# Optimization experiments

Measured on AMD Instinct MI355X. Metric: run time of the kernel, lower is better.

## Reference

```python
import jax, jax.numpy as jnp
import numpy as np

N, E, G, D, H = 50000, 800000, 64, 64, 256  # nodes, edges, graphs, feat dim, mlp hidden


def _mlp(x, W1, b1, W2, b2):
    return jax.nn.relu(x @ W1 + b1) @ W2 + b2


def _param(key, fan_in, fan_out):
    return jax.random.normal(key, (fan_in, fan_out), dtype=jnp.float32) * (1.0 / np.sqrt(fan_in))


def setup_inputs() -> dict:
    key = jax.random.key(0)
    ks = jax.random.split(key, 16)
    inp = {
        "nf": jax.random.normal(ks[0], (N, D), dtype=jnp.float32),
        "ef": jax.random.normal(ks[1], (E, D), dtype=jnp.float32),
        "u": jax.random.normal(ks[2], (G, D), dtype=jnp.float32),
        "src": jax.random.randint(ks[3], (E,), 0, N, dtype=jnp.int32),
        "dst": jax.random.randint(ks[4], (E,), 0, N, dtype=jnp.int32),
        "node_gid": jnp.sort(jax.random.randint(ks[5], (N,), 0, G, dtype=jnp.int32)),
        "edge_gid": jnp.sort(jax.random.randint(ks[6], (E,), 0, G, dtype=jnp.int32)),
        # edge_model: in = De + 2*Dn + Du = 4D
        "eW1": _param(ks[7], 4 * D, H), "eb1": jnp.zeros((H,), jnp.float32),
        "eW2": _param(ks[8], H, D),     "eb2": jnp.zeros((D,), jnp.float32),
        # node_model: in = De + Dn + Du = 3D
        "nW1": _param(ks[9], 3 * D, H), "nb1": jnp.zeros((H,), jnp.float32),
        "nW2": _param(ks[10], H, D),    "nb2": jnp.zeros((D,), jnp.float32),
        # global_model: in = De + Dn + Du = 3D
        "gW1": _param(ks[11], 3 * D, H), "gb1": jnp.zeros((H,), jnp.float32),
        "gW2": _param(ks[12], H, D),     "gb2": jnp.zeros((D,), jnp.float32),
    }
    return inp


def reference(nf, ef, u, src, dst, node_gid, edge_gid,
              eW1, eb1, eW2, eb2, nW1, nb1, nW2, nb2, gW1, gb1, gW2, gb2):
    # --- edge update: cat([ef, src_nf, dst_nf, u_per_edge]) -> edge MLP ---
    u_e = u[edge_gid]                                   # [E, D] (repeat_interleave by batch_num_edges)
    em_in = jnp.concatenate([ef, nf[src], nf[dst], u_e], axis=-1)  # [E, 4D]
    ef_new = _mlp(em_in, eW1, eb1, eW2, eb2)            # [E, D]

    # --- message = copy_e, reduce = sum at destination nodes ---
    agg_m = jax.ops.segment_sum(ef_new, dst, num_segments=N)       # [N, D]

    # --- node update: cat([agg_m, nf, u_per_node]) -> node MLP ---
    u_n = u[node_gid]                                   # [N, D]
    nm_in = jnp.concatenate([agg_m, nf, u_n], axis=-1)  # [N, 3D]
    nf_new = _mlp(nm_in, nW1, nb1, nW2, nb2)            # [N, D]

    # --- global update: per-graph sum readouts of updated edge/node feats ---
    e_aggr = jax.ops.segment_sum(ef_new, edge_gid, num_segments=G)  # [G, D]
    n_aggr = jax.ops.segment_sum(nf_new, node_gid, num_segments=G)  # [G, D]
    gm_in = jnp.concatenate([e_aggr, n_aggr, u], axis=-1)           # [G, 3D]
    u_new = _mlp(gm_in, gW1, gb1, gW2, gb2)             # [G, D]

    return nf_new, ef_new, u_new
```

## Files before the change

### kernel.cpp

```cpp
#include <hip/hip_runtime.h>
#include <stdint.h>
#include <stddef.h>

#define NN 50000
#define EE 800000
#define GG 64
#define DD 64
#define HH 256

typedef float f32x4 __attribute__((ext_vector_type(4)));
typedef short s16x8 __attribute__((ext_vector_type(8)));
typedef short s16x4 __attribute__((ext_vector_type(4)));

__device__ __forceinline__ short f2bf(float f) {
    union { float f; unsigned u; } v; v.f = f;
    return (short)((v.u + 0x7FFFu + ((v.u >> 16) & 1u)) >> 16);
}

__global__ void prep_weights(const float* __restrict__ eW1, const float* __restrict__ eW2,
                             const float* __restrict__ nW1, const float* __restrict__ nW2,
                             short* __restrict__ W1t, short* __restrict__ W2t,
                             short* __restrict__ NW1t, short* __restrict__ NW2t) {
    int idx = blockIdx.x * blockDim.x + threadIdx.x;
    {
        int n = idx >> 8, k = idx & 255;
        W1t[idx] = f2bf(eW1[k * 256 + n]);
    }
    if (idx < 49152) {
        int n = idx / 192, k = idx - n * 192;
        NW1t[idx] = f2bf(nW1[k * 256 + n]);
    }
    if (idx < 16384) {
        int n = idx >> 8, k = idx & 255;
        W2t[idx]  = f2bf(eW2[k * 64 + n]);
        NW2t[idx] = f2bf(nW2[k * 64 + n]);
    }
}

#define SA1 264
#define SAN 200

__global__ __launch_bounds__(256, 4) void edge_kernel(
    const float* __restrict__ nf, const float* __restrict__ ef, const float* __restrict__ u,
    const int* __restrict__ src, const int* __restrict__ dst, const int* __restrict__ egid,
    const short* __restrict__ W1t, const float* __restrict__ b1,
    const short* __restrict__ W2t, const float* __restrict__ b2,
    float* __restrict__ ef_new, float* __restrict__ agg_m, float* __restrict__ e_aggr)
{
    __shared__ __align__(16) short As[64 * SA1];
    __shared__ int dstS[64];
    __shared__ int gidS[64];
    __shared__ float redS[4][64];

    const int t = threadIdx.x;
    const int e0 = blockIdx.x * 64;
    const int wave = t >> 6, lane = t & 63;
    const int l15 = lane & 15, lq = lane >> 4;

    int idxv;
    if (wave == 0)      idxv = e0 + lane;
    else if (wave == 1) idxv = src[e0 + lane];
    else if (wave == 2) { idxv = dst[e0 + lane]; dstS[lane] = idxv; }
    else                { idxv = egid[e0 + lane]; gidS[lane] = idxv; }

    const float* segbase = (wave == 0) ? ef : (wave == 3) ? u : nf;

    {
        const int rsub = lane >> 4;
        const int c4 = (lane & 15) * 4;
        #pragma unroll
        for (int r = 0; r < 16; ++r) {
            const int row = r * 4 + rsub;
            const float* sp = segbase + (size_t)__shfl(idxv, row) * 64 + c4;
            f32x4 v = *(const f32x4*)sp;
            s16x4 h = { f2bf(v.x), f2bf(v.y), f2bf(v.z), f2bf(v.w) };
            *(s16x4*)(As + row * SA1 + wave * 64 + c4) = h;
        }
    }
    __syncthreads();

    f32x4 acc[4][4] = {};
    const short* aB = As + l15 * SA1 + lq * 8;
    const short* bB = W1t + (size_t)(wave * 64 + l15) * 256 + lq * 8;
    #pragma unroll
    for (int kk = 0; kk < 8; ++kk) {
        s16x8 a[4], b[4];
        #pragma unroll
        for (int rt = 0; rt < 4; ++rt) a[rt] = *(const s16x8*)(aB + rt * 16 * SA1 + kk * 32);
        #pragma unroll
        for (int ct = 0; ct < 4; ++ct) b[ct] = *(const s16x8*)(bB + (size_t)ct * 16 * 256 + kk * 32);
        #pragma unroll
        for (int rt = 0; rt < 4; ++rt)
            #pragma unroll
            for (int ct = 0; ct < 4; ++ct)
                acc[rt][ct] = __builtin_amdgcn_mfma_f32_16x16x32_bf16(a[rt], b[ct], acc[rt][ct], 0, 0, 0);
    }
    __syncthreads();

    #pragma unroll
    for (int ct = 0; ct < 4; ++ct) {
        int col = wave * 64 + ct * 16 + l15;
        float bb = b1[col];
        #pragma unroll
        for (int rt = 0; rt < 4; ++rt)
            #pragma unroll
            for (int r = 0; r < 4; ++r) {
                int rr = rt * 16 + lq * 4 + r;
                float v = acc[rt][ct][r] + bb;
                As[rr * SA1 + col] = f2bf(v > 0.f ? v : 0.f);
            }
    }
    __syncthreads();

    f32x4 acc2[4] = {};
    const short* aB2 = As + l15 * SA1 + lq * 8;
    const short* bB2 = W2t + (size_t)(wave * 16 + l15) * 256 + lq * 8;
    #pragma unroll
    for (int kk = 0; kk < 8; ++kk) {
        s16x8 b = *(const s16x8*)(bB2 + kk * 32);
        #pragma unroll
        for (int rt = 0; rt < 4; ++rt) {
            s16x8 a = *(const s16x8*)(aB2 + rt * 16 * SA1 + kk * 32);
            acc2[rt] = __builtin_amdgcn_mfma_f32_16x16x32_bf16(a, b, acc2[rt], 0, 0, 0);
        }
    }
    __syncthreads();

    float* Y2s = (float*)As;
    {
        const int colo = wave * 16 + l15;
        const float bo = b2[colo];
        #pragma unroll
        for (int rt = 0; rt < 4; ++rt)
            #pragma unroll
            for (int r = 0; r < 4; ++r) {
                int rr = rt * 16 + lq * 4 + r;
                Y2s[rr * 65 + colo] = acc2[rt][r] + bo;
            }
    }
    __syncthreads();

    const bool uni = (gidS[0] == gidS[63]);
    float ps = 0.f;
    #pragma unroll
    for (int r = 0; r < 16; ++r) {
        int row = wave * 16 + r;
        float v = Y2s[row * 65 + lane];
        __builtin_nontemporal_store(v, &ef_new[(size_t)(e0 + row) * 64 + lane]);
        atomicAdd(&agg_m[(size_t)dstS[row] * 64 + lane], v);
        ps += v;
    }
    if (uni) redS[wave][lane] = ps;
    __syncthreads();

    if (uni) {
        if (wave == 0) {
            float s = redS[0][lane] + redS[1][lane] + redS[2][lane] + redS[3][lane];
            atomicAdd(&e_aggr[gidS[0] * 64 + lane], s);
        }
    } else if (t < 64) {
        float sum = 0.f; int g = gidS[0];
        for (int rr = 0; rr < 64; ++rr) {
            int gg = gidS[rr];
            if (gg != g) { atomicAdd(&e_aggr[g * 64 + t], sum); sum = 0.f; g = gg; }
            sum += Y2s[rr * 65 + t];
        }
        atomicAdd(&e_aggr[g * 64 + t], sum);
    }
}

__global__ __launch_bounds__(256, 2) void node_kernel(
    const float* __restrict__ nf, const float* __restrict__ u,
    const int* __restrict__ ngid, const float* __restrict__ agg_m,
    const short* __restrict__ W1t, const float* __restrict__ b1,
    const short* __restrict__ W2t, const float* __restrict__ b2,
    float* __restrict__ nf_new, float* __restrict__ n_aggr)
{
    __shared__ __align__(16) short As[64 * SA1];
    __shared__ int gidS[64];

    const int t = threadIdx.x;
    const int n0 = blockIdx.x * 64;

    {
        const int row = t >> 2, q = t & 3;
        const int i = n0 + row;
        const bool valid = i < NN;
        int g = valid ? ngid[i] : -1;
        if (q == 0) gidS[row] = g;
        short* arow = As + row * SAN;
        if (valid) {
            #pragma unroll
            for (int c4 = q * 48; c4 < q * 48 + 48; c4 += 4) {
                int seg = c4 >> 6, off = c4 & 63;
                const float* p = (seg == 0) ? (agg_m + (size_t)i * 64 + off)
                              : (seg == 1) ? (nf + (size_t)i * 64 + off)
                                           : (u + (size_t)g * 64 + off);
                f32x4 v = *(const f32x4*)p;
                s16x4 h = { f2bf(v.x), f2bf(v.y), f2bf(v.z), f2bf(v.w) };
                *(s16x4*)(arow + c4) = h;
            }
        } else {
            s16x4 z = {0, 0, 0, 0};
            #pragma unroll
            for (int c4 = q * 48; c4 < q * 48 + 48; c4 += 4)
                *(s16x4*)(arow + c4) = z;
        }
    }
    __syncthreads();

    const int wave = t >> 6, lane = t & 63;
    const int l15 = lane & 15, lq = lane >> 4;

    f32x4 acc[4][4] = {};
    const short* aB = As + l15 * SAN + lq * 8;
    const short* bB = W1t + (size_t)(wave * 64 + l15) * 192 + lq * 8;
    #pragma unroll
    for (int kk = 0; kk < 6; ++kk) {
        s16x8 a[4], b[4];
        #pragma unroll
        for (int rt = 0; rt < 4; ++rt) a[rt] = *(const s16x8*)(aB + rt * 16 * SAN + kk * 32);
        #pragma unroll
        for (int ct = 0; ct < 4; ++ct) b[ct] = *(const s16x8*)(bB + (size_t)ct * 16 * 192 + kk * 32);
        #pragma unroll
        for (int rt = 0; rt < 4; ++rt)
            #pragma unroll
            for (int ct = 0; ct < 4; ++ct)
                acc[rt][ct] = __builtin_amdgcn_mfma_f32_16x16x32_bf16(a[rt], b[ct], acc[rt][ct], 0, 0, 0);
    }
    __syncthreads();

    #pragma unroll
    for (int ct = 0; ct < 4; ++ct) {
        int col = wave * 64 + ct * 16 + l15;
        float bb = b1[col];
        #pragma unroll
        for (int rt = 0; rt < 4; ++rt)
            #pragma unroll
            for (int r = 0; r < 4; ++r) {
                int rr = rt * 16 + lq * 4 + r;
                float v = acc[rt][ct][r] + bb;
                As[rr * SA1 + col] = f2bf(v > 0.f ? v : 0.f);
            }
    }
    __syncthreads();

    f32x4 acc2[4] = {};
    const short* aB2 = As + l15 * SA1 + lq * 8;
    const short* bB2 = W2t + (size_t)(wave * 16 + l15) * 256 + lq * 8;
    #pragma unroll
    for (int kk = 0; kk < 8; ++kk) {
        s16x8 b = *(const s16x8*)(bB2 + kk * 32);
        #pragma unroll
        for (int rt = 0; rt < 4; ++rt) {
            s16x8 a = *(const s16x8*)(aB2 + rt * 16 * SA1 + kk * 32);
            acc2[rt] = __builtin_amdgcn_mfma_f32_16x16x32_bf16(a, b, acc2[rt], 0, 0, 0);
        }
    }
    __syncthreads();

    float* Y2s = (float*)As;
    const int colo = wave * 16 + l15;
    const float bo = b2[colo];
    #pragma unroll
    for (int rt = 0; rt < 4; ++rt)
        #pragma unroll
        for (int r = 0; r < 4; ++r) {
            int rr = rt * 16 + lq * 4 + r;
            float v = acc2[rt][r] + bo;
            bool ok = (n0 + rr) < NN;
            if (ok) nf_new[(size_t)(n0 + rr) * 64 + colo] = v;
            Y2s[rr * 65 + colo] = ok ? v : 0.f;
        }
    __syncthreads();

    if (t < 64) {
        float sum = 0.f; int g = gidS[0];
        for (int rr = 0; rr < 64; ++rr) {
            int gg = gidS[rr];
            if (gg != g) {
                if (g >= 0) atomicAdd(&n_aggr[g * 64 + t], sum);
                sum = 0.f; g = gg;
            }
            sum += Y2s[rr * 65 + t];
        }
        if (g >= 0) atomicAdd(&n_aggr[g * 64 + t], sum);
    }
}

__global__ void global_kernel(const float* __restrict__ e_aggr, const float* __restrict__ n_aggr,
                              const float* __restrict__ u,
                              const float* __restrict__ gW1, const float* __restrict__ gb1,
                              const float* __restrict__ gW2, const float* __restrict__ gb2,
                              float* __restrict__ u_new)
{
    __shared__ float gin[192];
    __shared__ float hid[256];
    const int g = blockIdx.x, t = threadIdx.x;
    if (t < 64)       gin[t] = e_aggr[g * 64 + t];
    else if (t < 128) gin[t] = n_aggr[g * 64 + (t - 64)];
    else if (t < 192) gin[t] = u[g * 64 + (t - 128)];
    __syncthreads();
    float s = gb1[t];
    #pragma unroll 8
    for (int k = 0; k < 192; ++k) s += gin[k] * gW1[k * 256 + t];
    hid[t] = s > 0.f ? s : 0.f;
    __syncthreads();
    if (t < 64) {
        float o = gb2[t];
        #pragma unroll 8
        for (int k = 0; k < 256; ++k) o += hid[k] * gW2[k * 64 + t];
        u_new[g * 64 + t] = o;
    }
}

#define WS_AGGM_OFF   0u
#define WS_AGGM_BYTES (NN * 64u * 4u)
#define WS_EAGG_OFF   (WS_AGGM_OFF + WS_AGGM_BYTES)
#define WS_NAGG_OFF   (WS_EAGG_OFF + GG * 64u * 4u)
#define WS_ZERO_BYTES (WS_NAGG_OFF + GG * 64u * 4u)
#define WS_W1T_OFF    WS_ZERO_BYTES
#define WS_W2T_OFF    (WS_W1T_OFF + 65536u * 2u)
#define WS_NW1T_OFF   (WS_W2T_OFF + 16384u * 2u)
#define WS_NW2T_OFF   (WS_NW1T_OFF + 49152u * 2u)

extern "C" void kernel_launch(void* const* d_in, const int* in_sizes, int n_in,
                              void* d_out, int out_size, void* d_ws, size_t ws_size,
                              hipStream_t stream) {
    const float* nf  = (const float*)d_in[0];
    const float* ef  = (const float*)d_in[1];
    const float* u   = (const float*)d_in[2];
    const int* src   = (const int*)d_in[3];
    const int* dst   = (const int*)d_in[4];
    const int* ngid  = (const int*)d_in[5];
    const int* egid  = (const int*)d_in[6];
    const float* eW1 = (const float*)d_in[7];
    const float* eb1 = (const float*)d_in[8];
    const float* eW2 = (const float*)d_in[9];
    const float* eb2 = (const float*)d_in[10];
    const float* nW1 = (const float*)d_in[11];
    const float* nb1 = (const float*)d_in[12];
    const float* nW2 = (const float*)d_in[13];
    const float* nb2 = (const float*)d_in[14];
    const float* gW1 = (const float*)d_in[15];
    const float* gb1 = (const float*)d_in[16];
    const float* gW2 = (const float*)d_in[17];
    const float* gb2 = (const float*)d_in[18];

    float* out    = (float*)d_out;
    float* nf_new = out;
    float* ef_new = out + (size_t)NN * DD;
    float* u_new  = out + (size_t)(NN + EE) * DD;

    char* ws = (char*)d_ws;
    float* agg_m  = (float*)(ws + WS_AGGM_OFF);
    float* e_aggr = (float*)(ws + WS_EAGG_OFF);
    float* n_aggr = (float*)(ws + WS_NAGG_OFF);
    short* W1t    = (short*)(ws + WS_W1T_OFF);
    short* W2t    = (short*)(ws + WS_W2T_OFF);
    short* NW1t   = (short*)(ws + WS_NW1T_OFF);
    short* NW2t   = (short*)(ws + WS_NW2T_OFF);

    hipMemsetAsync(d_ws, 0, WS_ZERO_BYTES, stream);
    prep_weights<<<256, 256, 0, stream>>>(eW1, eW2, nW1, nW2, W1t, W2t, NW1t, NW2t);
    edge_kernel<<<EE / 64, 256, 0, stream>>>(nf, ef, u, src, dst, egid,
                                             W1t, eb1, W2t, eb2, ef_new, agg_m, e_aggr);
    node_kernel<<<(NN + 63) / 64, 256, 0, stream>>>(nf, u, ngid, agg_m,
                                                    NW1t, nb1, NW2t, nb2, nf_new, n_aggr);
    global_kernel<<<GG, 256, 0, stream>>>(e_aggr, n_aggr, u, gW1, gb1, gW2, gb2, u_new);
}
```

Before: 720.6 us.

## Make edge kernel persistent with register prefetch of next tile's gathers

The edge kernel becomes persistent (512 blocks, grid-stride over 64-edge tiles). It holds W2 fragments and biases in registers and prefetches the next tile's gathered feature rows into registers while the current tile's MLP runs, using a separate LDS buffer for hidden activations. The node kernel gets coalesced row-wise loads, a wave-reduced per-graph readout when a block's nodes share one graph, and a higher occupancy hint. This hides gather latency behind MFMA work, at the cost of more registers and LDS per block and lower occupancy for the edge kernel.

```diff
diff --git a/kernel.cpp b/kernel.cpp
--- a/kernel.cpp
+++ b/kernel.cpp
@@ -15,6 +15,11 @@
 __device__ __forceinline__ short f2bf(float f) {
     union { float f; unsigned u; } v; v.f = f;
     return (short)((v.u + 0x7FFFu + ((v.u >> 16) & 1u)) >> 16);
+}
+
+__device__ __forceinline__ s16x4 f2bf4(f32x4 v) {
+    s16x4 h = { f2bf(v.x), f2bf(v.y), f2bf(v.z), f2bf(v.w) };
+    return h;
 }
 
 __global__ void prep_weights(const float* __restrict__ eW1, const float* __restrict__ eW2,
@@ -40,7 +45,7 @@
 #define SA1 264
 #define SAN 200
 
-__global__ __launch_bounds__(256, 4) void edge_kernel(
+__global__ __launch_bounds__(256, 2) void edge_kernel(
     const float* __restrict__ nf, const float* __restrict__ ef, const float* __restrict__ u,
     const int* __restrict__ src, const int* __restrict__ dst, const int* __restrict__ egid,
     const short* __restrict__ W1t, const float* __restrict__ b1,
@@ -48,128 +53,172 @@
     float* __restrict__ ef_new, float* __restrict__ agg_m, float* __restrict__ e_aggr)
 {
     __shared__ __align__(16) short As[64 * SA1];
+    __shared__ __align__(16) short Y1s[64 * SA1];
     __shared__ int dstS[64];
     __shared__ int gidS[64];
     __shared__ float redS[4][64];
 
     const int t = threadIdx.x;
-    const int e0 = blockIdx.x * 64;
     const int wave = t >> 6, lane = t & 63;
     const int l15 = lane & 15, lq = lane >> 4;
-
-    int idxv;
-    if (wave == 0)      idxv = e0 + lane;
-    else if (wave == 1) idxv = src[e0 + lane];
-    else if (wave == 2) { idxv = dst[e0 + lane]; dstS[lane] = idxv; }
-    else                { idxv = egid[e0 + lane]; gidS[lane] = idxv; }
+    const int rsub = lane >> 4;
+    const int c4l = (lane & 15) * 4;
+    const int NB64 = gridDim.x * 64;
 
     const float* segbase = (wave == 0) ? ef : (wave == 3) ? u : nf;
 
+    s16x8 w2f[8];
     {
-        const int rsub = lane >> 4;
-        const int c4 = (lane & 15) * 4;
-        #pragma unroll
-        for (int r = 0; r < 16; ++r) {
-            const int row = r * 4 + rsub;
-            const float* sp = segbase + (size_t)__shfl(idxv, row) * 64 + c4;
-            f32x4 v = *(const f32x4*)sp;
-            s16x4 h = { f2bf(v.x), f2bf(v.y), f2bf(v.z), f2bf(v.w) };
-            *(s16x4*)(As + row * SA1 + wave * 64 + c4) = h;
-        }
-    }
-    __syncthreads();
-
-    f32x4 acc[4][4] = {};
-    const short* aB = As + l15 * SA1 + lq * 8;
-    const short* bB = W1t + (size_t)(wave * 64 + l15) * 256 + lq * 8;
+        const short* bB2 = W2t + (size_t)(wave * 16 + l15) * 256 + lq * 8;
+        #pragma unroll
+        for (int kk = 0; kk < 8; ++kk) w2f[kk] = *(const s16x8*)(bB2 + kk * 32);
+    }
+    float bias1[4];
     #pragma unroll
-    for (int kk = 0; kk < 8; ++kk) {
-        s16x8 a[4], b[4];
-        #pragma unroll
-        for (int rt = 0; rt < 4; ++rt) a[rt] = *(const s16x8*)(aB + rt * 16 * SA1 + kk * 32);
-        #pragma unroll
-        for (int ct = 0; ct < 4; ++ct) b[ct] = *(const s16x8*)(bB + (size_t)ct * 16 * 256 + kk * 32);
-        #pragma unroll
-        for (int rt = 0; rt < 4; ++rt)
-            #pragma unroll
-            for (int ct = 0; ct < 4; ++ct)
-                acc[rt][ct] = __builtin_amdgcn_mfma_f32_16x16x32_bf16(a[rt], b[ct], acc[rt][ct], 0, 0, 0);
-    }
-    __syncthreads();
-
-    #pragma unroll
-    for (int ct = 0; ct < 4; ++ct) {
-        int col = wave * 64 + ct * 16 + l15;
-        float bb = b1[col];
-        #pragma unroll
-        for (int rt = 0; rt < 4; ++rt)
-            #pragma unroll
-            for (int r = 0; r < 4; ++r) {
-                int rr = rt * 16 + lq * 4 + r;
-                float v = acc[rt][ct][r] + bb;
-                As[rr * SA1 + col] = f2bf(v > 0.f ? v : 0.f);
-            }
-    }
-    __syncthreads();
-
-    f32x4 acc2[4] = {};
-    const short* aB2 = As + l15 * SA1 + lq * 8;
-    const short* bB2 = W2t + (size_t)(wave * 16 + l15) * 256 + lq * 8;
-    #pragma unroll
-    for (int kk = 0; kk < 8; ++kk) {
-        s16x8 b = *(const s16x8*)(bB2 + kk * 32);
-        #pragma unroll
-        for (int rt = 0; rt < 4; ++rt) {
-            s16x8 a = *(const s16x8*)(aB2 + rt * 16 * SA1 + kk * 32);
-            acc2[rt] = __builtin_amdgcn_mfma_f32_16x16x32_bf16(a, b, acc2[rt], 0, 0, 0);
-        }
-    }
-    __syncthreads();
-
-    float* Y2s = (float*)As;
-    {
-        const int colo = wave * 16 + l15;
-        const float bo = b2[colo];
-        #pragma unroll
-        for (int rt = 0; rt < 4; ++rt)
-            #pragma unroll
-            for (int r = 0; r < 4; ++r) {
-                int rr = rt * 16 + lq * 4 + r;
-                Y2s[rr * 65 + colo] = acc2[rt][r] + bo;
-            }
-    }
-    __syncthreads();
-
-    const bool uni = (gidS[0] == gidS[63]);
-    float ps = 0.f;
+    for (int ct = 0; ct < 4; ++ct) bias1[ct] = b1[wave * 64 + ct * 16 + l15];
+    const float bo = b2[wave * 16 + l15];
+
+    int e0 = blockIdx.x * 64;
+    int idxc;
+    f32x4 pf[16];
+    if (wave == 0)      idxc = e0 + lane;
+    else if (wave == 1) idxc = src[e0 + lane];
+    else if (wave == 2) idxc = dst[e0 + lane];
+    else                idxc = egid[e0 + lane];
     #pragma unroll
     for (int r = 0; r < 16; ++r) {
-        int row = wave * 16 + r;
-        float v = Y2s[row * 65 + lane];
-        __builtin_nontemporal_store(v, &ef_new[(size_t)(e0 + row) * 64 + lane]);
-        atomicAdd(&agg_m[(size_t)dstS[row] * 64 + lane], v);
-        ps += v;
-    }
-    if (uni) redS[wave][lane] = ps;
-    __syncthreads();
-
-    if (uni) {
-        if (wave == 0) {
-            float s = redS[0][lane] + redS[1][lane] + redS[2][lane] + redS[3][lane];
-            atomicAdd(&e_aggr[gidS[0] * 64 + lane], s);
-        }
-    } else if (t < 64) {
-        float sum = 0.f; int g = gidS[0];
-        for (int rr = 0; rr < 64; ++rr) {
-            int gg = gidS[rr];
-            if (gg != g) { atomicAdd(&e_aggr[g * 64 + t], sum); sum = 0.f; g = gg; }
-            sum += Y2s[rr * 65 + t];
-        }
-        atomicAdd(&e_aggr[g * 64 + t], sum);
-    }
-}
-
-__global__ __launch_bounds__(256, 2) void node_kernel(
+        int row = r * 4 + rsub;
+        pf[r] = *(const f32x4*)(segbase + (size_t)__shfl(idxc, row) * 64 + c4l);
+    }
+
+    for (; e0 < EE; e0 += NB64) {
+        const bool has_next = (e0 + NB64) < EE;
+
+        #pragma unroll
+        for (int r = 0; r < 16; ++r) {
+            int row = r * 4 + rsub;
+            *(s16x4*)(As + row * SA1 + wave * 64 + c4l) = f2bf4(pf[r]);
+        }
+        if (wave == 2)      dstS[lane] = idxc;
+        else if (wave == 3) gidS[lane] = idxc;
+        __syncthreads();
+
+        int idxn;
+        if (has_next) {
+            int e0n = e0 + NB64;
+            if (wave == 0)      idxn = e0n + lane;
+            else if (wave == 1) idxn = src[e0n + lane];
+            else if (wave == 2) idxn = dst[e0n + lane];
+            else                idxn = egid[e0n + lane];
+        }
+
+        f32x4 acc[4][4] = {};
+        {
+            const short* aB = As + l15 * SA1 + lq * 8;
+            const short* bB = W1t + (size_t)(wave * 64 + l15) * 256 + lq * 8;
+            #pragma unroll
+            for (int kk = 0; kk < 8; ++kk) {
+                s16x8 a[4], b[4];
+                #pragma unroll
+                for (int rt = 0; rt < 4; ++rt) a[rt] = *(const s16x8*)(aB + rt * 16 * SA1 + kk * 32);
+                #pragma unroll
+                for (int ct = 0; ct < 4; ++ct) b[ct] = *(const s16x8*)(bB + (size_t)ct * 16 * 256 + kk * 32);
+                #pragma unroll
+                for (int rt = 0; rt < 4; ++rt)
+                    #pragma unroll
+                    for (int ct = 0; ct < 4; ++ct)
+                        acc[rt][ct] = __builtin_amdgcn_mfma_f32_16x16x32_bf16(a[rt], b[ct], acc[rt][ct], 0, 0, 0);
+            }
+        }
+        __syncthreads();
+
+        #pragma unroll
+        for (int ct = 0; ct < 4; ++ct) {
+            int col = wave * 64 + ct * 16 + l15;
+            float bb = bias1[ct];
+            #pragma unroll
+            for (int rt = 0; rt < 4; ++rt)
+                #pragma unroll
+                for (int r = 0; r < 4; ++r) {
+                    int rr = rt * 16 + lq * 4 + r;
+                    float v = acc[rt][ct][r] + bb;
+                    Y1s[rr * SA1 + col] = f2bf(v > 0.f ? v : 0.f);
+                }
+        }
+
+        if (has_next) {
+            #pragma unroll
+            for (int r = 0; r < 16; ++r) {
+                int row = r * 4 + rsub;
+                pf[r] = *(const f32x4*)(segbase + (size_t)__shfl(idxn, row) * 64 + c4l);
+            }
+        }
+        __syncthreads();
+
+        f32x4 acc2[4] = {};
+        {
+            const short* aB2 = Y1s + l15 * SA1 + lq * 8;
+            #pragma unroll
+            for (int kk = 0; kk < 8; ++kk) {
+                #pragma unroll
+                for (int rt = 0; rt < 4; ++rt) {
+                    s16x8 a = *(const s16x8*)(aB2 + rt * 16 * SA1 + kk * 32);
+                    acc2[rt] = __builtin_amdgcn_mfma_f32_16x16x32_bf16(a, w2f[kk], acc2[rt], 0, 0, 0);
+                }
+            }
+        }
+        __syncthreads();
+
+        float* Y2s = (float*)Y1s;
+        {
+            const int colo = wave * 16 + l15;
+            #pragma unroll
+            for (int rt = 0; rt < 4; ++rt)
+                #pragma unroll
+                for (int r = 0; r < 4; ++r) {
+                    int rr = rt * 16 + lq * 4 + r;
+                    Y2s[rr * 65 + colo] = acc2[rt][r] + bo;
+                }
+        }
+        __syncthreads();
+
+        const bool uni = (gidS[0] == gidS[63]);
+        const int g0 = gidS[0];
+        float ps = 0.f;
+        #pragma unroll
+        for (int r = 0; r < 16; ++r) {
+            int row = wave * 16 + r;
+            float v = Y2s[row * 65 + lane];
+            __builtin_nontemporal_store(v, &ef_new[(size_t)(e0 + row) * 64 + lane]);
+            atomicAdd(&agg_m[(size_t)dstS[row] * 64 + lane], v);
+            ps += v;
+        }
+        if (uni) redS[wave][lane] = ps;
+        __syncthreads();
+
+        if (uni) {
+            if (wave == 0) {
+                float s = redS[0][lane] + redS[1][lane] + redS[2][lane] + redS[3][lane];
+                atomicAdd(&e_aggr[g0 * 64 + lane], s);
+            }
+        } else {
+            if (t < 64) {
+                float sum = 0.f; int g = gidS[0];
+                for (int rr = 0; rr < 64; ++rr) {
+                    int gg = gidS[rr];
+                    if (gg != g) { atomicAdd(&e_aggr[g * 64 + t], sum); sum = 0.f; g = gg; }
+                    sum += Y2s[rr * 65 + t];
+                }
+                atomicAdd(&e_aggr[g * 64 + t], sum);
+            }
+            __syncthreads();
+        }
+
+        if (has_next) idxc = idxn;
+    }
+}
+
+__global__ __launch_bounds__(256, 4) void node_kernel(
     const float* __restrict__ nf, const float* __restrict__ u,
     const int* __restrict__ ngid, const float* __restrict__ agg_m,
     const short* __restrict__ W1t, const float* __restrict__ b1,
@@ -178,34 +227,31 @@
 {
     __shared__ __align__(16) short As[64 * SA1];
     __shared__ int gidS[64];
+    __shared__ float redS[4][64];
 
     const int t = threadIdx.x;
     const int n0 = blockIdx.x * 64;
 
-    {
-        const int row = t >> 2, q = t & 3;
-        const int i = n0 + row;
-        const bool valid = i < NN;
-        int g = valid ? ngid[i] : -1;
-        if (q == 0) gidS[row] = g;
+    if (t < 64) gidS[t] = (n0 + t < NN) ? ngid[n0 + t] : -1;
+    __syncthreads();
+
+    #pragma unroll
+    for (int itq = 0; itq < 4; ++itq) {
+        int idx = itq * 256 + t;
+        int row = idx >> 4;
+        int c4 = (idx & 15) * 4;
+        bool valid = (n0 + row) < NN;
+        f32x4 va = {0.f, 0.f, 0.f, 0.f}, vb = va, vc = va;
+        if (valid) {
+            int g = gidS[row];
+            va = *(const f32x4*)(agg_m + (size_t)(n0 + row) * 64 + c4);
+            vb = *(const f32x4*)(nf + (size_t)(n0 + row) * 64 + c4);
+            vc = *(const f32x4*)(u + (size_t)g * 64 + c4);
+        }
         short* arow = As + row * SAN;
-        if (valid) {
-            #pragma unroll
-            for (int c4 = q * 48; c4 < q * 48 + 48; c4 += 4) {
-                int seg = c4 >> 6, off = c4 & 63;
-                const float* p = (seg == 0) ? (agg_m + (size_t)i * 64 + off)
-                              : (seg == 1) ? (nf + (size_t)i * 64 + off)
-                                           : (u + (size_t)g * 64 + off);
-                f32x4 v = *(const f32x4*)p;
-                s16x4 h = { f2bf(v.x), f2bf(v.y), f2bf(v.z), f2bf(v.w) };
-                *(s16x4*)(arow + c4) = h;
-            }
-        } else {
-            s16x4 z = {0, 0, 0, 0};
-            #pragma unroll
-            for (int c4 = q * 48; c4 < q * 48 + 48; c4 += 4)
-                *(s16x4*)(arow + c4) = z;
-        }
+        *(s16x4*)(arow + c4)        = f2bf4(va);
+        *(s16x4*)(arow + 64 + c4)   = f2bf4(vb);
+        *(s16x4*)(arow + 128 + c4)  = f2bf4(vc);
     }
     __syncthreads();
 
@@ -213,20 +259,22 @@
     const int l15 = lane & 15, lq = lane >> 4;
 
     f32x4 acc[4][4] = {};
-    const short* aB = As + l15 * SAN + lq * 8;
-    const short* bB = W1t + (size_t)(wave * 64 + l15) * 192 + lq * 8;
-    #pragma unroll
-    for (int kk = 0; kk < 6; ++kk) {
-        s16x8 a[4], b[4];
-        #pragma unroll
-        for (int rt = 0; rt < 4; ++rt) a[rt] = *(const s16x8*)(aB + rt * 16 * SAN + kk * 32);
-        #pragma unroll
-        for (int ct = 0; ct < 4; ++ct) b[ct] = *(const s16x8*)(bB + (size_t)ct * 16 * 192 + kk * 32);
-        #pragma unroll
-        for (int rt = 0; rt < 4; ++rt)
-            #pragma unroll
-            for (int ct = 0; ct < 4; ++ct)
-                acc[rt][ct] = __builtin_amdgcn_mfma_f32_16x16x32_bf16(a[rt], b[ct], acc[rt][ct], 0, 0, 0);
+    {
+        const short* aB = As + l15 * SAN + lq * 8;
+        const short* bB = W1t + (size_t)(wave * 64 + l15) * 192 + lq * 8;
+        #pragma unroll
+        for (int kk = 0; kk < 6; ++kk) {
+            s16x8 a[4], b[4];
+            #pragma unroll
+            for (int rt = 0; rt < 4; ++rt) a[rt] = *(const s16x8*)(aB + rt * 16 * SAN + kk * 32);
+            #pragma unroll
+            for (int ct = 0; ct < 4; ++ct) b[ct] = *(const s16x8*)(bB + (size_t)ct * 16 * 192 + kk * 32);
+            #pragma unroll
+            for (int rt = 0; rt < 4; ++rt)
+                #pragma unroll
+                for (int ct = 0; ct < 4; ++ct)
+                    acc[rt][ct] = __builtin_amdgcn_mfma_f32_16x16x32_bf16(a[rt], b[ct], acc[rt][ct], 0, 0, 0);
+        }
     }
     __syncthreads();
 
@@ -246,35 +294,55 @@
     __syncthreads();
 
     f32x4 acc2[4] = {};
-    const short* aB2 = As + l15 * SA1 + lq * 8;
-    const short* bB2 = W2t + (size_t)(wave * 16 + l15) * 256 + lq * 8;
+    {
+        const short* aB2 = As + l15 * SA1 + lq * 8;
+        const short* bB2 = W2t + (size_t)(wave * 16 + l15) * 256 + lq * 8;
+        #pragma unroll
+        for (int kk = 0; kk < 8; ++kk) {
+            s16x8 b = *(const s16x8*)(bB2 + kk * 32);
+            #pragma unroll
+            for (int rt = 0; rt < 4; ++rt) {
+                s16x8 a = *(const s16x8*)(aB2 + rt * 16 * SA1 + kk * 32);
+                acc2[rt] = __builtin_amdgcn_mfma_f32_16x16x32_bf16(a, b, acc2[rt], 0, 0, 0);
+            }
+        }
+    }
+    __syncthreads();
+
+    float* Y2s = (float*)As;
+    {
+        const int colo = wave * 16 + l15;
+        const float bo = b2[colo];
+        #pragma unroll
+        for (int rt = 0; rt < 4; ++rt)
+            #pragma unroll
+            for (int r = 0; r < 4; ++r) {
+                int rr = rt * 16 + lq * 4 + r;
+                float v = acc2[rt][r] + bo;
+                Y2s[rr * 65 + colo] = ((n0 + rr) < NN) ? v : 0.f;
+            }
+    }
+    __syncthreads();
+
+    const bool uni = (gidS[0] == gidS[63]) && (gidS[0] >= 0);
+    const int g0 = gidS[0];
+    float ps = 0.f;
     #pragma unroll
-    for (int kk = 0; kk < 8; ++kk) {
-        s16x8 b = *(const s16x8*)(bB2 + kk * 32);
-        #pragma unroll
-        for (int rt = 0; rt < 4; ++rt) {
-            s16x8 a = *(const s16x8*)(aB2 + rt * 16 * SA1 + kk * 32);
-            acc2[rt] = __builtin_amdgcn_mfma_f32_16x16x32_bf16(a, b, acc2[rt], 0, 0, 0);
-        }
-    }
-    __syncthreads();
-
-    float* Y2s = (float*)As;
-    const int colo = wave * 16 + l15;
-    const float bo = b2[colo];
-    #pragma unroll
-    for (int rt = 0; rt < 4; ++rt)
-        #pragma unroll
-        for (int r = 0; r < 4; ++r) {
-            int rr = rt * 16 + lq * 4 + r;
-            float v = acc2[rt][r] + bo;
-            bool ok = (n0 + rr) < NN;
-            if (ok) nf_new[(size_t)(n0 + rr) * 64 + colo] = v;
-            Y2s[rr * 65 + colo] = ok ? v : 0.f;
-        }
-    __syncthreads();
-
-    if (t < 64) {
+    for (int r = 0; r < 16; ++r) {
+        int row = wave * 16 + r;
+        float v = Y2s[row * 65 + lane];
+        if ((n0 + row) < NN) nf_new[(size_t)(n0 + row) * 64 + lane] = v;
+        ps += v;
+    }
+    if (uni) redS[wave][lane] = ps;
+    __syncthreads();
+
+    if (uni) {
+        if (wave == 0) {
+            float s = redS[0][lane] + redS[1][lane] + redS[2][lane] + redS[3][lane];
+            atomicAdd(&n_aggr[g0 * 64 + lane], s);
+        }
+    } else if (t < 64) {
         float sum = 0.f; int g = gidS[0];
         for (int rr = 0; rr < 64; ++rr) {
             int gg = gidS[rr];
@@ -363,8 +431,8 @@
 
     hipMemsetAsync(d_ws, 0, WS_ZERO_BYTES, stream);
     prep_weights<<<256, 256, 0, stream>>>(eW1, eW2, nW1, nW2, W1t, W2t, NW1t, NW2t);
-    edge_kernel<<<EE / 64, 256, 0, stream>>>(nf, ef, u, src, dst, egid,
-                                             W1t, eb1, W2t, eb2, ef_new, agg_m, e_aggr);
+    edge_kernel<<<512, 256, 0, stream>>>(nf, ef, u, src, dst, egid,
+                                         W1t, eb1, W2t, eb2, ef_new, agg_m, e_aggr);
     node_kernel<<<(NN + 63) / 64, 256, 0, stream>>>(nf, u, ngid, agg_m,
                                                     NW1t, nb1, NW2t, nb2, nf_new, n_aggr);
     global_kernel<<<GG, 256, 0, stream>>>(e_aggr, n_aggr, u, gW1, gb1, gW2, gb2, u_new);
```

Result: slower. 758.6 us (+5.3%).

## Pre-swizzle bf16 weights into MFMA fragment order and coalesce node kernel I/O

Applied to the files above, without the earlier changes.

The weight prep kernel now writes the bf16 weights in per-lane MFMA fragment order, so each wave reads its B operands as contiguous 512-element chunks (one 16-byte load per lane) instead of strided row reads. The node kernel gathers its inputs with row/column-coalesced float4 loads, writes nf_new row-contiguously from shared memory, and uses a uniform-graph fast path for the n_aggr reduction. Its launch bound rises to 4 blocks per CU. The result is cheaper global loads for weights and activations, at the cost of more complex index math in prep and extra register pressure from the higher occupancy target.

```diff
diff --git a/kernel.cpp b/kernel.cpp
--- a/kernel.cpp
+++ b/kernel.cpp
@@ -17,23 +17,37 @@
     return (short)((v.u + 0x7FFFu + ((v.u >> 16) & 1u)) >> 16);
 }
 
+__device__ __forceinline__ s16x4 f2bf4(f32x4 v) {
+    s16x4 h = { f2bf(v.x), f2bf(v.y), f2bf(v.z), f2bf(v.w) };
+    return h;
+}
+
 __global__ void prep_weights(const float* __restrict__ eW1, const float* __restrict__ eW2,
                              const float* __restrict__ nW1, const float* __restrict__ nW2,
-                             short* __restrict__ W1t, short* __restrict__ W2t,
-                             short* __restrict__ NW1t, short* __restrict__ NW2t) {
+                             short* __restrict__ W1f, short* __restrict__ W2f,
+                             short* __restrict__ NW1f, short* __restrict__ NW2f) {
     int idx = blockIdx.x * blockDim.x + threadIdx.x;
-    {
-        int n = idx >> 8, k = idx & 255;
-        W1t[idx] = f2bf(eW1[k * 256 + n]);
+    int lane = (idx >> 3) & 63, j = idx & 7;
+    int l15 = lane & 15, lq = lane >> 4;
+    {
+        int c = idx >> 9;
+        int n = (c >> 5) * 64 + ((c >> 3) & 3) * 16 + l15;
+        int k = lq * 8 + (c & 7) * 32 + j;
+        W1f[idx] = f2bf(eW1[k * 256 + n]);
     }
     if (idx < 49152) {
-        int n = idx / 192, k = idx - n * 192;
-        NW1t[idx] = f2bf(nW1[k * 256 + n]);
+        int c = idx >> 9;
+        int w = c / 24, r = c - w * 24;
+        int n = w * 64 + (r / 6) * 16 + l15;
+        int k = lq * 8 + (r % 6) * 32 + j;
+        NW1f[idx] = f2bf(nW1[k * 256 + n]);
     }
     if (idx < 16384) {
-        int n = idx >> 8, k = idx & 255;
-        W2t[idx]  = f2bf(eW2[k * 64 + n]);
-        NW2t[idx] = f2bf(nW2[k * 64 + n]);
+        int c = idx >> 9;
+        int n = (c >> 3) * 16 + l15;
+        int k = lq * 8 + (c & 7) * 32 + j;
+        W2f[idx]  = f2bf(eW2[k * 64 + n]);
+        NW2f[idx] = f2bf(nW2[k * 64 + n]);
     }
 }
 
@@ -43,8 +57,8 @@
 __global__ __launch_bounds__(256, 4) void edge_kernel(
     const float* __restrict__ nf, const float* __restrict__ ef, const float* __restrict__ u,
     const int* __restrict__ src, const int* __restrict__ dst, const int* __restrict__ egid,
-    const short* __restrict__ W1t, const float* __restrict__ b1,
-    const short* __restrict__ W2t, const float* __restrict__ b2,
+    const short* __restrict__ W1f, const float* __restrict__ b1,
+    const short* __restrict__ W2f, const float* __restrict__ b2,
     float* __restrict__ ef_new, float* __restrict__ agg_m, float* __restrict__ e_aggr)
 {
     __shared__ __align__(16) short As[64 * SA1];
@@ -73,22 +87,21 @@
             const int row = r * 4 + rsub;
             const float* sp = segbase + (size_t)__shfl(idxv, row) * 64 + c4;
             f32x4 v = *(const f32x4*)sp;
-            s16x4 h = { f2bf(v.x), f2bf(v.y), f2bf(v.z), f2bf(v.w) };
-            *(s16x4*)(As + row * SA1 + wave * 64 + c4) = h;
+            *(s16x4*)(As + row * SA1 + wave * 64 + c4) = f2bf4(v);
         }
     }
     __syncthreads();
 
     f32x4 acc[4][4] = {};
     const short* aB = As + l15 * SA1 + lq * 8;
-    const short* bB = W1t + (size_t)(wave * 64 + l15) * 256 + lq * 8;
+    const short* bB = W1f + (size_t)(wave * 32) * 512 + lane * 8;
     #pragma unroll
     for (int kk = 0; kk < 8; ++kk) {
         s16x8 a[4], b[4];
         #pragma unroll
         for (int rt = 0; rt < 4; ++rt) a[rt] = *(const s16x8*)(aB + rt * 16 * SA1 + kk * 32);
         #pragma unroll
-        for (int ct = 0; ct < 4; ++ct) b[ct] = *(const s16x8*)(bB + (size_t)ct * 16 * 256 + kk * 32);
+        for (int ct = 0; ct < 4; ++ct) b[ct] = *(const s16x8*)(bB + (ct * 8 + kk) * 512);
         #pragma unroll
         for (int rt = 0; rt < 4; ++rt)
             #pragma unroll
@@ -114,10 +127,10 @@
 
     f32x4 acc2[4] = {};
     const short* aB2 = As + l15 * SA1 + lq * 8;
-    const short* bB2 = W2t + (size_t)(wave * 16 + l15) * 256 + lq * 8;
+    const short* bB2 = W2f + (size_t)(wave * 8) * 512 + lane * 8;
     #pragma unroll
     for (int kk = 0; kk < 8; ++kk) {
-        s16x8 b = *(const s16x8*)(bB2 + kk * 32);
+        s16x8 b = *(const s16x8*)(bB2 + kk * 512);
         #pragma unroll
         for (int rt = 0; rt < 4; ++rt) {
             s16x8 a = *(const s16x8*)(aB2 + rt * 16 * SA1 + kk * 32);
@@ -141,6 +154,7 @@
     __syncthreads();
 
     const bool uni = (gidS[0] == gidS[63]);
+    const int g0 = gidS[0];
     float ps = 0.f;
     #pragma unroll
     for (int r = 0; r < 16; ++r) {
@@ -156,7 +170,7 @@
     if (uni) {
         if (wave == 0) {
             float s = redS[0][lane] + redS[1][lane] + redS[2][lane] + redS[3][lane];
-            atomicAdd(&e_aggr[gidS[0] * 64 + lane], s);
+            atomicAdd(&e_aggr[g0 * 64 + lane], s);
         }
     } else if (t < 64) {
         float sum = 0.f; int g = gidS[0];
@@ -169,43 +183,40 @@
     }
 }
 
-__global__ __launch_bounds__(256, 2) void node_kernel(
+__global__ __launch_bounds__(256, 4) void node_kernel(
     const float* __restrict__ nf, const float* __restrict__ u,
     const int* __restrict__ ngid, const float* __restrict__ agg_m,
-    const short* __restrict__ W1t, const float* __restrict__ b1,
-    const short* __restrict__ W2t, const float* __restrict__ b2,
+    const short* __restrict__ W1f, const float* __restrict__ b1,
+    const short* __restrict__ W2f, const float* __restrict__ b2,
     float* __restrict__ nf_new, float* __restrict__ n_aggr)
 {
     __shared__ __align__(16) short As[64 * SA1];
     __shared__ int gidS[64];
+    __shared__ float redS[4][64];
 
     const int t = threadIdx.x;
     const int n0 = blockIdx.x * 64;
 
-    {
-        const int row = t >> 2, q = t & 3;
-        const int i = n0 + row;
-        const bool valid = i < NN;
-        int g = valid ? ngid[i] : -1;
-        if (q == 0) gidS[row] = g;
+    if (t < 64) gidS[t] = (n0 + t < NN) ? ngid[n0 + t] : -1;
+    __syncthreads();
+
+    #pragma unroll
+    for (int itq = 0; itq < 4; ++itq) {
+        int idx = itq * 256 + t;
+        int row = idx >> 4;
+        int c4 = (idx & 15) * 4;
+        bool valid = (n0 + row) < NN;
+        f32x4 va = {0.f, 0.f, 0.f, 0.f}, vb = va, vc = va;
+        if (valid) {
+            int g = gidS[row];
+            va = *(const f32x4*)(agg_m + (size_t)(n0 + row) * 64 + c4);
+            vb = *(const f32x4*)(nf + (size_t)(n0 + row) * 64 + c4);
+            vc = *(const f32x4*)(u + (size_t)g * 64 + c4);
+        }
         short* arow = As + row * SAN;
-        if (valid) {
-            #pragma unroll
-            for (int c4 = q * 48; c4 < q * 48 + 48; c4 += 4) {
-                int seg = c4 >> 6, off = c4 & 63;
-                const float* p = (seg == 0) ? (agg_m + (size_t)i * 64 + off)
-                              : (seg == 1) ? (nf + (size_t)i * 64 + off)
-                                           : (u + (size_t)g * 64 + off);
-                f32x4 v = *(const f32x4*)p;
-                s16x4 h = { f2bf(v.x), f2bf(v.y), f2bf(v.z), f2bf(v.w) };
-                *(s16x4*)(arow + c4) = h;
-            }
-        } else {
-            s16x4 z = {0, 0, 0, 0};
-            #pragma unroll
-            for (int c4 = q * 48; c4 < q * 48 + 48; c4 += 4)
-                *(s16x4*)(arow + c4) = z;
-        }
+        *(s16x4*)(arow + c4)        = f2bf4(va);
+        *(s16x4*)(arow + 64 + c4)   = f2bf4(vb);
+        *(s16x4*)(arow + 128 + c4)  = f2bf4(vc);
     }
     __syncthreads();
 
@@ -213,20 +224,22 @@
     const int l15 = lane & 15, lq = lane >> 4;
 
     f32x4 acc[4][4] = {};
-    const short* aB = As + l15 * SAN + lq * 8;
-    const short* bB = W1t + (size_t)(wave * 64 + l15) * 192 + lq * 8;
-    #pragma unroll
-    for (int kk = 0; kk < 6; ++kk) {
-        s16x8 a[4], b[4];
-        #pragma unroll
-        for (int rt = 0; rt < 4; ++rt) a[rt] = *(const s16x8*)(aB + rt * 16 * SAN + kk * 32);
-        #pragma unroll
-        for (int ct = 0; ct < 4; ++ct) b[ct] = *(const s16x8*)(bB + (size_t)ct * 16 * 192 + kk * 32);
-        #pragma unroll
-        for (int rt = 0; rt < 4; ++rt)
-            #pragma unroll
-            for (int ct = 0; ct < 4; ++ct)
-                acc[rt][ct] = __builtin_amdgcn_mfma_f32_16x16x32_bf16(a[rt], b[ct], acc[rt][ct], 0, 0, 0);
+    {
+        const short* aB = As + l15 * SAN + lq * 8;
+        const short* bB = W1f + (size_t)(wave * 24) * 512 + lane * 8;
+        #pragma unroll
+        for (int kk = 0; kk < 6; ++kk) {
+            s16x8 a[4], b[4];
+            #pragma unroll
+            for (int rt = 0; rt < 4; ++rt) a[rt] = *(const s16x8*)(aB + rt * 16 * SAN + kk * 32);
+            #pragma unroll
+            for (int ct = 0; ct < 4; ++ct) b[ct] = *(const s16x8*)(bB + (ct * 6 + kk) * 512);
+            #pragma unroll
+            for (int rt = 0; rt < 4; ++rt)
+                #pragma unroll
+                for (int ct = 0; ct < 4; ++ct)
+                    acc[rt][ct] = __builtin_amdgcn_mfma_f32_16x16x32_bf16(a[rt], b[ct], acc[rt][ct], 0, 0, 0);
+        }
     }
     __syncthreads();
 
@@ -246,35 +259,55 @@
     __syncthreads();
 
     f32x4 acc2[4] = {};
-    const short* aB2 = As + l15 * SA1 + lq * 8;
-    const short* bB2 = W2t + (size_t)(wave * 16 + l15) * 256 + lq * 8;
-    #pragma unroll
-    for (int kk = 0; kk < 8; ++kk) {
-        s16x8 b = *(const s16x8*)(bB2 + kk * 32);
-        #pragma unroll
-        for (int rt = 0; rt < 4; ++rt) {
-            s16x8 a = *(const s16x8*)(aB2 + rt * 16 * SA1 + kk * 32);
-            acc2[rt] = __builtin_amdgcn_mfma_f32_16x16x32_bf16(a, b, acc2[rt], 0, 0, 0);
+    {
+        const short* aB2 = As + l15 * SA1 + lq * 8;
+        const short* bB2 = W2f + (size_t)(wave * 8) * 512 + lane * 8;
+        #pragma unroll
+        for (int kk = 0; kk < 8; ++kk) {
+            s16x8 b = *(const s16x8*)(bB2 + kk * 512);
+            #pragma unroll
+            for (int rt = 0; rt < 4; ++rt) {
+                s16x8 a = *(const s16x8*)(aB2 + rt * 16 * SA1 + kk * 32);
+                acc2[rt] = __builtin_amdgcn_mfma_f32_16x16x32_bf16(a, b, acc2[rt], 0, 0, 0);
+            }
         }
     }
     __syncthreads();
 
     float* Y2s = (float*)As;
-    const int colo = wave * 16 + l15;
-    const float bo = b2[colo];
-    #pragma unroll
-    for (int rt = 0; rt < 4; ++rt)
-        #pragma unroll
-        for (int r = 0; r < 4; ++r) {
-            int rr = rt * 16 + lq * 4 + r;
-            float v = acc2[rt][r] + bo;
-            bool ok = (n0 + rr) < NN;
-            if (ok) nf_new[(size_t)(n0 + rr) * 64 + colo] = v;
-            Y2s[rr * 65 + colo] = ok ? v : 0.f;
-        }
-    __syncthreads();
-
-    if (t < 64) {
+    {
+        const int colo = wave * 16 + l15;
+        const float bo = b2[colo];
+        #pragma unroll
+        for (int rt = 0; rt < 4; ++rt)
+            #pragma unroll
+            for (int r = 0; r < 4; ++r) {
+                int rr = rt * 16 + lq * 4 + r;
+                float v = acc2[rt][r] + bo;
+                Y2s[rr * 65 + colo] = ((n0 + rr) < NN) ? v : 0.f;
+            }
+    }
+    __syncthreads();
+
+    const bool uni = (gidS[0] == gidS[63]) && (gidS[0] >= 0);
+    const int g0 = gidS[0];
+    float ps = 0.f;
+    #pragma unroll
+    for (int r = 0; r < 16; ++r) {
+        int row = wave * 16 + r;
+        float v = Y2s[row * 65 + lane];
+        if ((n0 + row) < NN) nf_new[(size_t)(n0 + row) * 64 + lane] = v;
+        ps += v;
+    }
+    if (uni) redS[wave][lane] = ps;
+    __syncthreads();
+
+    if (uni) {
+        if (wave == 0) {
+            float s = redS[0][lane] + redS[1][lane] + redS[2][lane] + redS[3][lane];
+            atomicAdd(&n_aggr[g0 * 64 + lane], s);
+        }
+    } else if (t < 64) {
         float sum = 0.f; int g = gidS[0];
         for (int rr = 0; rr < 64; ++rr) {
             int gg = gidS[rr];
@@ -356,16 +389,16 @@
     float* agg_m  = (float*)(ws + WS_AGGM_OFF);
     float* e_aggr = (float*)(ws + WS_EAGG_OFF);
     float* n_aggr = (float*)(ws + WS_NAGG_OFF);
-    short* W1t    = (short*)(ws + WS_W1T_OFF);
-    short* W2t    = (short*)(ws + WS_W2T_OFF);
-    short* NW1t   = (short*)(ws + WS_NW1T_OFF);
-    short* NW2t   = (short*)(ws + WS_NW2T_OFF);
+    short* W1f    = (short*)(ws + WS_W1T_OFF);
+    short* W2f    = (short*)(ws + WS_W2T_OFF);
+    short* NW1f   = (short*)(ws + WS_NW1T_OFF);
+    short* NW2f   = (short*)(ws + WS_NW2T_OFF);
 
     hipMemsetAsync(d_ws, 0, WS_ZERO_BYTES, stream);
-    prep_weights<<<256, 256, 0, stream>>>(eW1, eW2, nW1, nW2, W1t, W2t, NW1t, NW2t);
+    prep_weights<<<256, 256, 0, stream>>>(eW1, eW2, nW1, nW2, W1f, W2f, NW1f, NW2f);
     edge_kernel<<<EE / 64, 256, 0, stream>>>(nf, ef, u, src, dst, egid,
-                                             W1t, eb1, W2t, eb2, ef_new, agg_m, e_aggr);
+                                             W1f, eb1, W2f, eb2, ef_new, agg_m, e_aggr);
     node_kernel<<<(NN + 63) / 64, 256, 0, stream>>>(nf, u, ngid, agg_m,
-                                                    NW1t, nb1, NW2t, nb2, nf_new, n_aggr);
+                                                    NW1f, nb1, NW2f, nb2, nf_new, n_aggr);
     global_kernel<<<GG, 256, 0, stream>>>(e_aggr, n_aggr, u, gW1, gb1, gW2, gb2, u_new);
 }
```

Measured after the change: 630.9 us. 12.4% less time.
